# Kernel tuning notes

Measured on AMD Instinct MI355X. Metric: run time of the kernel, lower is better.

## Reference

```python
import jax, jax.numpy as jnp
import numpy as np

N_DIS = 5000
N_GEN = 20000
N = N_DIS + N_GEN
E = 400000
N_MIRNA = 2000
EMB = 128
HID = 64


def setup_inputs() -> dict:
    key = jax.random.key(0)
    ks = jax.random.split(key, 20)
    def g(k, shape, scale=0.05):
        return jax.random.normal(k, shape, dtype=jnp.float32) * scale
    return {
        'd_features': g(ks[0], (N_DIS, 383), 1.0),
        'g_features': g(ks[1], (N_GEN, 4395), 1.0),
        'miRNA_dis': jax.random.uniform(ks[2], (N_MIRNA, N_DIS), dtype=jnp.float32),
        'gene_dis': jax.random.uniform(ks[3], (N_GEN, N_DIS), dtype=jnp.float32),
        'Wd': g(ks[4], (383, EMB)),
        'bd': jnp.zeros((EMB,), jnp.float32),
        'Wg': g(ks[5], (4395, EMB)),
        'bg': jnp.zeros((EMB,), jnp.float32),
        'W1': g(ks[6], (N_MIRNA, EMB)),
        'W4': g(ks[7], (N_DIS, EMB)),
        'Ws1': g(ks[8], (EMB, HID)),
        'Wn1': g(ks[9], (EMB, HID)),
        'b1': jnp.zeros((HID,), jnp.float32),
        'Ws2': g(ks[10], (HID, HID)),
        'Wn2': g(ks[11], (HID, HID)),
        'b2': jnp.zeros((HID,), jnp.float32),
        'src': jax.random.randint(ks[12], (E,), 0, N, dtype=jnp.int32),
        'dst': jax.random.randint(ks[13], (E,), 0, N, dtype=jnp.int32),
    }


def _sage_mean(h, src, dst, Ws, Wn, b):
    # DGL SAGEConv 'mean': fc_self(h) + fc_neigh(mean over in-neighbors) + bias
    msg = h[src]                                            # [E, d] gather
    agg = jax.ops.segment_sum(msg, dst, num_segments=N)     # [N, d] scatter-add
    deg = jax.ops.segment_sum(jnp.ones((dst.shape[0],), h.dtype), dst, num_segments=N)
    neigh = agg / jnp.maximum(deg, 1.0)[:, None]            # mean (zero-deg -> 0)
    return h @ Ws + neigh @ Wn + b


def reference(d_features, g_features, miRNA_dis, gene_dis, Wd, bd, Wg, bg,
              W1, W4, Ws1, Wn1, b1, Ws2, Wn2, b2, src, dst):
    # CrossCompressUnit outputs used by forward: A2 = M1^T W1, B1 = M2 W4
    A2 = miRNA_dis.T @ W1          # [N_DIS, EMB]
    B1 = gene_dis @ W4             # [N_GEN, EMB]
    # Node embeddings (dropout is identity at inference; torch.no_grad block)
    h_dis = 0.9 * (d_features @ Wd + bd) + 0.1 * A2   # [N_DIS, EMB]
    h_gen = 0.9 * (g_features @ Wg + bg) + 0.1 * B1   # [N_GEN, EMB]
    h = jnp.concatenate([h_dis, h_gen], axis=0)        # [N, EMB]
    h = _sage_mean(h, src, dst, Ws1, Wn1, b1)          # [N, 64]
    h = jax.nn.relu(h)
    h = _sage_mean(h, src, dst, Ws2, Wn2, b2)          # [N, 64]
    return h
```

## Files before the change

kernel.cpp:

```cpp
#include <hip/hip_runtime.h>

#define NDIS 5000
#define NGEN 20000
#define NTOT 25000
#define EDG  400000

typedef __attribute__((ext_vector_type(8))) short short8;
typedef __attribute__((ext_vector_type(4))) float f32x4;
typedef __attribute__((ext_vector_type(4), aligned(4))) float f32x4u;
typedef __attribute__((ext_vector_type(4))) unsigned int uint4v;
typedef __attribute__((ext_vector_type(2))) unsigned int uint2v;
typedef __attribute__((ext_vector_type(2), aligned(4))) unsigned int uint2a;

constexpr size_t AL(size_t x) { return (x + 255) & ~(size_t)255; }
constexpr size_t OFF_H0   = 0;
constexpr size_t OFF_PQ   = AL(OFF_H0  + (size_t)NTOT * 128 * 4);
constexpr size_t OFF_H1   = AL(OFF_PQ  + (size_t)NTOT * 128 * 4);
constexpr size_t OFF_DEG  = AL(OFF_H1  + (size_t)NTOT * 128 * 4);
constexpr size_t OFF_RS   = AL(OFF_DEG + (size_t)NTOT * 4);
constexpr size_t OFF_CUR  = AL(OFF_RS  + (size_t)(NTOT + 1) * 4);
constexpr size_t OFF_TMP  = AL(OFF_CUR + (size_t)NTOT * 4);
constexpr size_t OFF_BSUM = AL(OFF_TMP + (size_t)NTOT * 4);
constexpr size_t OFF_BOFF = AL(OFF_BSUM + 64 * 4);
constexpr size_t OFF_ESRC = AL(OFF_BOFF + 64 * 4);
constexpr size_t OFF_MIT  = AL(OFF_ESRC + (size_t)EDG * 4);
constexpr size_t OFF_BDIS = AL(OFF_MIT + (size_t)5000 * 2048 * 2);
constexpr size_t OFF_BGEN = AL(OFF_BDIS + (size_t)8 * 76 * 512 * 2);
constexpr size_t OFF_BS1  = AL(OFF_BGEN + (size_t)8 * 300 * 512 * 2);
constexpr size_t OFF_BS2  = AL(OFF_BS1 + (size_t)8 * 4 * 512 * 2);

__device__ __forceinline__ ushort f2bf(float f) {
    unsigned u = __float_as_uint(f);
    u += 0x7fffu + ((u >> 16) & 1u);
    return (ushort)(u >> 16);
}

__device__ __forceinline__ unsigned cvtpk(float a, float b) {
    unsigned r;
    asm("v_cvt_pk_bf16_f32 %0, %1, %2" : "=v"(r) : "v"(a), "v"(b));
    return r;
}

__device__ __forceinline__ void MFMA(f32x4& d, short8 a, short8 b) {
    asm volatile("v_mfma_f32_16x16x32_bf16 %0, %1, %2, %0"
                 : "+v"(d) : "v"(a), "v"(b));
}

struct TcvtIns { const float* p[9]; };

__global__ __launch_bounds__(256) void k_tcvt_multi(TcvtIns ins, char* ws,
                                                    const int* __restrict__ dst,
                                                    int* __restrict__ deg)
{
    constexpr int   TR[9]   = {383, 2000, 4395, 5000, 2000, 128, 128, 64, 64};
    constexpr int   TC[9]   = {128, 128, 128, 128, 5000, 64, 64, 64, 64};
    constexpr int   TKT[9]  = {76, 76, 300, 300, 2048 , 4, 4, 4, 4};
    constexpr int   TKO[9]  = {0, 12, 0, 140, 0, 0, 0, 0, 0};
    constexpr int   TRP[9]  = {384, 2048, 4480, 5120, 2048, 128, 128, 128, 128};
    constexpr int   TNOFF[9]= {0, 0, 0, 0, 0, 0, 64, 0, 64};
    constexpr int   TMODE[9]= {1, 1, 1, 1, 0, 1, 1, 1, 1};
    constexpr float TSC[9]  = {0.9f, 0.1f, 0.9f, 0.1f, 1.f, 1.f, 1.f, 1.f, 1.f};
    constexpr size_t TOUT[9]= {OFF_BDIS, OFF_BDIS, OFF_BGEN, OFF_BGEN, OFF_MIT,
                               OFF_BS1, OFF_BS1, OFF_BS2, OFF_BS2};
    constexpr int TNBX[9]   = {4, 4, 4, 4, 157, 2, 2, 2, 2};
    constexpr int PRE[10]   = {0, 48, 304, 864, 1504, 11552, 11560, 11568, 11576, 11584};

    int bid = blockIdx.x;
    if (bid >= 11584) {
        int e = (bid - 11584) * 256 + threadIdx.x;
        if (e < EDG) atomicAdd(&deg[dst[e]], 1);
        return;
    }
    int d = 0;
#pragma unroll
    for (int q = 1; q < 9; ++q) if (bid >= PRE[q]) d = q;
    int local = bid - PRE[d];
    int bx = local % TNBX[d], by = local / TNBX[d];
    const int R = TR[d], C = TC[d], KT = TKT[d], KO = TKO[d];
    const int Rp = TRP[d], noff = TNOFF[d];
    const float scale = TSC[d];
    const float* in = ins.p[d];
    ushort* out = (ushort*)(ws + TOUT[d]);

    __shared__ float t[32][33];
    int tx = threadIdx.x & 31, ty = threadIdx.x >> 5;
    int c0 = bx * 32, r0 = by * 32;
#pragma unroll
    for (int j = 0; j < 4; ++j) {
        int r = r0 + ty + j * 8, c = c0 + tx;
        t[ty + j * 8][tx] = (r < R && c < C) ? in[(size_t)r * C + c] : 0.f;
    }
    __syncthreads();
#pragma unroll
    for (int j = 0; j < 4; ++j) {
        int c = c0 + ty + j * 8, r = r0 + tx;
        if (c >= C || r >= Rp) continue;
        ushort bv = f2bf(scale * t[tx][ty + j * 8]);
        if (TMODE[d] == 0) {
            out[(size_t)c * KT + r] = bv;
        } else {
            int n = noff + c, k = r;
            out[(size_t)((n >> 4) * KT + KO + (k >> 5)) * 512 +
                ((k >> 3) & 3) * 128 + (n & 15) * 8 + (k & 7)] = bv;
        }
    }
}

template<int A2MODE, bool ATOMIC>
__global__ __launch_bounds__(256, 2) void gemm_st(
    const float* __restrict__ A1, int lda1, int K1, int nst1,
    const void* __restrict__ A2v, int lda2, int K2, int nst2,
    const ushort* __restrict__ Bf, int KT,
    float* __restrict__ C, int M, const float* __restrict__ bias)
{
    __shared__ ushort lds0[64 * 128];
    __shared__ ushort lds1[64 * 128];
    const int tid  = threadIdx.x;
    const int lane = tid & 63;
    const int w    = tid >> 6;
    const int fr = lane & 15, kq = lane >> 4;
    const int bm0 = blockIdx.x * 64;

    const int NSTT = nst1 + nst2;
    const int per = (NSTT + gridDim.y - 1) / gridDim.y;
    const int s0 = blockIdx.y * per;
    const int s1 = min(NSTT, s0 + per);
    const int NT = s1 - s0;
    if (NT <= 0) return;

    f32x4 acc[4][2];
#pragma unroll
    for (int i = 0; i < 4; ++i) { acc[i][0] = {0.f,0.f,0.f,0.f}; acc[i][1] = {0.f,0.f,0.f,0.f}; }

    uint4v faA[8], faB[8];
    short8 Breg0[4][2], Breg1[4][2];

    const int srow = w * 16 + (lane >> 5);
    const int scol = lane & 31;

    auto issueA = [&](int stg, uint4v* fa) {
        const bool r1 = (A2MODE == 0) || (stg < nst1);
#pragma unroll
        for (int i = 0; i < 8; ++i) {
            int r = bm0 + srow + i * 2;
            if (r > M - 1) r = M - 1;
            if (r1) {
                const int kb = stg << 7;
                const int k = kb + scol * 4;
                const float* p = A1 + (size_t)r * lda1 + k;
                if (kb + 128 <= K1) {
                    fa[i] = __builtin_bit_cast(uint4v, *(const f32x4u*)p);
                } else {
                    f32x4 v;
#pragma unroll
                    for (int e = 0; e < 4; ++e) v[e] = (k + e < K1) ? p[e] : 0.f;
                    fa[i] = __builtin_bit_cast(uint4v, v);
                }
            } else if (A2MODE == 1) {
                const int kb = (stg - nst1) << 7;
                const int kc = kb + scol * 4;
                const float* p = (const float*)A2v + (size_t)r * lda2 + kc;
                if (kb + 128 <= K2) {
                    fa[i] = __builtin_bit_cast(uint4v, *(const f32x4u*)p);
                } else {
                    f32x4 v;
#pragma unroll
                    for (int e = 0; e < 4; ++e) v[e] = (kc + e < K2) ? p[e] : 0.f;
                    fa[i] = __builtin_bit_cast(uint4v, v);
                }
            } else {
                const int kc = ((stg - nst1) << 7) + scol * 4;
                uint2a v = *(const uint2a*)((const ushort*)A2v + (size_t)r * lda2 + kc);
                fa[i][0] = v[0]; fa[i][1] = v[1];
            }
        }
    };
    auto issueB = [&](int stg, short8 (*BR)[2]) {
#pragma unroll
        for (int ks = 0; ks < 4; ++ks)
#pragma unroll
            for (int nf = 0; nf < 2; ++nf)
                BR[ks][nf] = *(const short8*)(
                    Bf + (size_t)((w * 2 + nf) * KT + stg * 4 + ks) * 512 + lane * 8);
    };
    auto writeT = [&](int stg, const uint4v* fa, ushort* buf) {
        const bool cvt = (A2MODE != 2) || (stg < nst1);
        const int G = scol >> 1, h = lane & 1;
#pragma unroll
        for (int i = 0; i < 8; ++i) {
            int r = srow + i * 2;
            const size_t off = (size_t)r * 256 + ((G ^ (r & 7)) << 4) + h * 8;
            uint2v d;
            if (cvt) {
                f32x4 v = __builtin_bit_cast(f32x4, fa[i]);
                d[0] = cvtpk(v[0], v[1]);
                d[1] = cvtpk(v[2], v[3]);
            } else {
                d[0] = fa[i][0]; d[1] = fa[i][1];
            }
            *(uint2v*)((char*)buf + off) = d;
        }
    };

#define PHASE(T, BR, LDSC, FAW, LDSW)                                        \
    {                                                                        \
        const int x7 = fr & 7;                                               \
        _Pragma("unroll")                                                    \
        for (int ks = 0; ks < 4; ++ks) {                                     \
            short8 af[4];                                                    \
            _Pragma("unroll")                                                \
            for (int mf = 0; mf < 4; ++mf)                                   \
                af[mf] = *(const short8*)&LDSC[fr * 128 + mf * 2048 +        \
                                              (((ks * 4 + kq) ^ x7) << 3)];  \
            _Pragma("unroll")                                                \
            for (int mf = 0; mf < 4; ++mf) {                                 \
                MFMA(acc[mf][0], af[mf], BR[ks][0]);                         \
                MFMA(acc[mf][1], af[mf], BR[ks][1]);                         \
            }                                                                \
        }                                                                    \
        if ((T) + 2 < NT) issueB(s0 + (T) + 2, BR);                          \
        __builtin_amdgcn_s_barrier();                                        \
        if ((T) + 1 < NT) {                                                  \
            writeT(s0 + (T) + 1, FAW, LDSW);                                 \
            if ((T) + 3 < NT) issueA(s0 + (T) + 3, FAW);                     \
            asm volatile("s_waitcnt lgkmcnt(0)" ::: "memory");               \
            __builtin_amdgcn_s_barrier();                                    \
        }                                                                    \
    }

    issueA(s0, faA); issueB(s0, Breg0);
    if (NT > 1) { issueA(s0 + 1, faB); issueB(s0 + 1, Breg1); }
    writeT(s0, faA, lds0);
    if (NT > 2) issueA(s0 + 2, faA);
    asm volatile("s_waitcnt lgkmcnt(0)" ::: "memory");
    __builtin_amdgcn_s_barrier();

    for (int t = 0; t < NT; t += 2) {
        PHASE(t, Breg0, lds0, faB, lds1);
        if (t + 1 < NT) PHASE(t + 1, Breg1, lds1, faA, lds0);
    }
#undef PHASE

    asm volatile("s_nop 7\n\ts_nop 7\n\ts_nop 7" ::: "memory");
#pragma unroll
    for (int mf = 0; mf < 4; ++mf)
#pragma unroll
        for (int nf = 0; nf < 2; ++nf)
#pragma unroll
            for (int r = 0; r < 4; ++r) {
                int row = bm0 + mf * 16 + kq * 4 + r;
                if (row < M) {
                    int col = w * 32 + nf * 16 + fr;
                    if (ATOMIC) {
                        atomicAdd(&C[(size_t)row * 128 + col], acc[mf][nf][r]);
                    } else {
                        float v = acc[mf][nf][r];
                        if (col < 64) v += bias[col];
                        C[(size_t)row * 128 + col] = v;
                    }
                }
            }
}

__global__ void k_binit(float* __restrict__ h0, const float* __restrict__ bd,
                        const float* __restrict__ bg) {
    int i = blockIdx.x * 256 + threadIdx.x;
    if (i >= NTOT * 128) return;
    int col = i & 127;
    h0[i] = 0.9f * ((i >> 7) < NDIS ? bd[col] : bg[col]);
}

__global__ __launch_bounds__(1024) void k_scan1(const int* __restrict__ deg,
                                                int* __restrict__ tmp,
                                                int* __restrict__ bsum, int n) {
    __shared__ int wsum[16];
    int t = threadIdx.x, lane = t & 63, wid = t >> 6;
    int i = blockIdx.x * 1024 + t;
    int v = (i < n) ? deg[i] : 0;
    int x = v;
#pragma unroll
    for (int off = 1; off < 64; off <<= 1) {
        int y = __shfl_up(x, off, 64);
        if (lane >= off) x += y;
    }
    if (lane == 63) wsum[wid] = x;
    __syncthreads();
    if (wid == 0) {
        int s = (lane < 16) ? wsum[lane] : 0;
#pragma unroll
        for (int off = 1; off < 16; off <<= 1) {
            int y = __shfl_up(s, off, 64);
            if (lane >= off) s += y;
        }
        if (lane < 16) wsum[lane] = s;
    }
    __syncthreads();
    int incl = x + (wid > 0 ? wsum[wid - 1] : 0);
    if (i < n) tmp[i] = incl;
    if (t == 1023) bsum[blockIdx.x] = incl;
}

__global__ void k_scan2(const int* __restrict__ bsum, int* __restrict__ boff, int nb) {
    int t = threadIdx.x;
    int v = (t < nb) ? bsum[t] : 0;
    int x = v;
#pragma unroll
    for (int off = 1; off < 64; off <<= 1) {
        int y = __shfl_up(x, off, 64);
        if (t >= off) x += y;
    }
    if (t < nb) boff[t] = x - v;
}

__global__ __launch_bounds__(1024) void k_scan3(const int* __restrict__ deg,
                                                const int* __restrict__ tmp,
                                                const int* __restrict__ boff,
                                                int* __restrict__ rs,
                                                int* __restrict__ cursor, int n) {
    int i = blockIdx.x * 1024 + threadIdx.x;
    if (i == 0) rs[0] = 0;
    if (i < n) {
        int v = tmp[i] + boff[blockIdx.x];
        rs[i + 1] = v;
        cursor[i] = v - deg[i];
    }
}

__global__ void k_fill(const int* __restrict__ src, const int* __restrict__ dst,
                       int* __restrict__ cursor, int* __restrict__ esrc, int E) {
    int e = blockIdx.x * blockDim.x + threadIdx.x;
    if (e < E) {
        int pos = atomicAdd(&cursor[dst[e]], 1);
        esrc[pos] = src[e];
    }
}

__global__ __launch_bounds__(64) void k_agg(const float* __restrict__ PQ,
                                            const int* __restrict__ rs,
                                            const int* __restrict__ esrc,
                                            float* __restrict__ out, int ldout, int relu)
{
    int n = blockIdx.x, t = threadIdx.x;
    int s0 = rs[n], s1 = rs[n + 1];
    float a0 = 0.f, a1 = 0.f, a2 = 0.f, a3 = 0.f;
    int i = s0;
    for (; i + 4 <= s1; i += 4) {
        int e0 = esrc[i], e1 = esrc[i + 1], e2 = esrc[i + 2], e3 = esrc[i + 3];
        a0 += PQ[(size_t)e0 * 128 + 64 + t];
        a1 += PQ[(size_t)e1 * 128 + 64 + t];
        a2 += PQ[(size_t)e2 * 128 + 64 + t];
        a3 += PQ[(size_t)e3 * 128 + 64 + t];
    }
    for (; i < s1; ++i) a0 += PQ[(size_t)esrc[i] * 128 + 64 + t];
    float s = (a0 + a1) + (a2 + a3);
    float dg = (float)(s1 - s0);
    s /= fmaxf(dg, 1.f);
    float v = PQ[(size_t)n * 128 + t] + s;
    if (relu) v = fmaxf(v, 0.f);
    out[(size_t)n * ldout + t] = v;
}

extern "C" void kernel_launch(void* const* d_in, const int* in_sizes, int n_in,
                              void* d_out, int out_size, void* d_ws, size_t ws_size,
                              hipStream_t stream)
{
    const float* d_features = (const float*)d_in[0];
    const float* g_features = (const float*)d_in[1];
    const float* miRNA_dis  = (const float*)d_in[2];
    const float* gene_dis   = (const float*)d_in[3];
    const float* Wd  = (const float*)d_in[4];
    const float* bd  = (const float*)d_in[5];
    const float* Wg  = (const float*)d_in[6];
    const float* bg  = (const float*)d_in[7];
    const float* W1  = (const float*)d_in[8];
    const float* W4  = (const float*)d_in[9];
    const float* Ws1 = (const float*)d_in[10];
    const float* Wn1 = (const float*)d_in[11];
    const float* b1  = (const float*)d_in[12];
    const float* Ws2 = (const float*)d_in[13];
    const float* Wn2 = (const float*)d_in[14];
    const float* b2  = (const float*)d_in[15];
    const int* src = (const int*)d_in[16];
    const int* dst = (const int*)d_in[17];
    (void)in_sizes; (void)n_in; (void)out_size; (void)ws_size;

    char* ws = (char*)d_ws;
    float*  h0   = (float*)(ws + OFF_H0);
    float*  PQ   = (float*)(ws + OFF_PQ);
    float*  h1   = (float*)(ws + OFF_H1);
    int*    deg  = (int*)(ws + OFF_DEG);
    int*    rs   = (int*)(ws + OFF_RS);
    int*    cur  = (int*)(ws + OFF_CUR);
    int*    tmp  = (int*)(ws + OFF_TMP);
    int*    bsum = (int*)(ws + OFF_BSUM);
    int*    boff = (int*)(ws + OFF_BOFF);
    int*    esrc = (int*)(ws + OFF_ESRC);
    ushort* miT  = (ushort*)(ws + OFF_MIT);
    ushort* Bdis = (ushort*)(ws + OFF_BDIS);
    ushort* Bgen = (ushort*)(ws + OFF_BGEN);
    ushort* Bs1  = (ushort*)(ws + OFF_BS1);
    ushort* Bs2  = (ushort*)(ws + OFF_BS2);

    hipMemsetAsync(deg, 0, (size_t)NTOT * 4, stream);
    hipMemsetAsync(h1, 0, (size_t)NTOT * 128 * 4, stream);

    TcvtIns ins;
    ins.p[0] = Wd;  ins.p[1] = W1;  ins.p[2] = Wg;  ins.p[3] = W4;
    ins.p[4] = miRNA_dis; ins.p[5] = Ws1; ins.p[6] = Wn1; ins.p[7] = Ws2; ins.p[8] = Wn2;
    k_tcvt_multi<<<11584 + 1563, 256, 0, stream>>>(ins, ws, dst, deg);

    k_scan1<<<25, 1024, 0, stream>>>(deg, tmp, bsum, NTOT);
    k_scan2<<<1, 64, 0, stream>>>(bsum, boff, 25);
    k_scan3<<<25, 1024, 0, stream>>>(deg, tmp, boff, rs, cur, NTOT);
    k_fill<<<(EDG + 255) / 256, 256, 0, stream>>>(src, dst, cur, esrc, EDG);

    k_binit<<<(NTOT * 128 + 255) / 256, 256, 0, stream>>>(h0, bd, bg);
    gemm_st<2, true><<<dim3(79, 5), 256, 0, stream>>>(
        d_features, 383, 383, 3,
        miT, 2048, 2048, 16, Bdis, 76, h0, NDIS, nullptr);
    gemm_st<1, true><<<dim3(313, 4), 256, 0, stream>>>(
        g_features, 4395, 4395, 35,
        gene_dis, 5000, 5000, 40, Bgen, 300,
        h0 + (size_t)NDIS * 128, NGEN, nullptr);

    gemm_st<0, false><<<dim3(391, 1), 256, 0, stream>>>(
        h0, 128, 128, 1, nullptr, 0, 0, 0, Bs1, 4, PQ, NTOT, b1);
    k_agg<<<NTOT, 64, 0, stream>>>(PQ, rs, esrc, h1, 128, 1);

    gemm_st<0, false><<<dim3(391, 1), 256, 0, stream>>>(
        h1, 128, 128, 1, nullptr, 0, 0, 0, Bs2, 4, PQ, NTOT, b2);
    k_agg<<<NTOT, 64, 0, stream>>>(PQ, rs, esrc, (float*)d_out, 64, 0);
}
```

Measured before the change: 351.6 us.

## Double GEMM K-stage depth and replace double-buffered LDS pipeline with single buffer

The GEMM kernel now takes a templated K-step count, so the big feature GEMMs process 256-wide K stages (half as many barriers and stages), with the B-fragment packing and padding widened to match. The ping-pong LDS buffers and two-deep prefetch are replaced by a single LDS buffer with a simpler load–write–compute loop that prefetches only one stage ahead. This trims per-stage synchronisation overhead and LDS footprint, but it loses the explicit overlap of global loads with compute, needs more registers for the wider prefetch, and pads more zero K columns.

```diff
diff --git a/kernel.cpp b/kernel.cpp
--- a/kernel.cpp
+++ b/kernel.cpp
@@ -25,8 +25,8 @@
 constexpr size_t OFF_ESRC = AL(OFF_BOFF + 64 * 4);
 constexpr size_t OFF_MIT  = AL(OFF_ESRC + (size_t)EDG * 4);
 constexpr size_t OFF_BDIS = AL(OFF_MIT + (size_t)5000 * 2048 * 2);
-constexpr size_t OFF_BGEN = AL(OFF_BDIS + (size_t)8 * 76 * 512 * 2);
-constexpr size_t OFF_BS1  = AL(OFF_BGEN + (size_t)8 * 300 * 512 * 2);
+constexpr size_t OFF_BGEN = AL(OFF_BDIS + (size_t)8 * 80 * 512 * 2);
+constexpr size_t OFF_BS1  = AL(OFF_BGEN + (size_t)8 * 304 * 512 * 2);
 constexpr size_t OFF_BS2  = AL(OFF_BS1 + (size_t)8 * 4 * 512 * 2);
 
 __device__ __forceinline__ ushort f2bf(float f) {
@@ -54,20 +54,20 @@
 {
     constexpr int   TR[9]   = {383, 2000, 4395, 5000, 2000, 128, 128, 64, 64};
     constexpr int   TC[9]   = {128, 128, 128, 128, 5000, 64, 64, 64, 64};
-    constexpr int   TKT[9]  = {76, 76, 300, 300, 2048 , 4, 4, 4, 4};
-    constexpr int   TKO[9]  = {0, 12, 0, 140, 0, 0, 0, 0, 0};
-    constexpr int   TRP[9]  = {384, 2048, 4480, 5120, 2048, 128, 128, 128, 128};
+    constexpr int   TKT[9]  = {80, 80, 304, 304, 2048 , 4, 4, 4, 4};
+    constexpr int   TKO[9]  = {0, 16, 0, 144, 0, 0, 0, 0, 0};
+    constexpr int   TRP[9]  = {512, 2048, 4608, 5120, 2048, 128, 128, 128, 128};
     constexpr int   TNOFF[9]= {0, 0, 0, 0, 0, 0, 64, 0, 64};
     constexpr int   TMODE[9]= {1, 1, 1, 1, 0, 1, 1, 1, 1};
     constexpr float TSC[9]  = {0.9f, 0.1f, 0.9f, 0.1f, 1.f, 1.f, 1.f, 1.f, 1.f};
     constexpr size_t TOUT[9]= {OFF_BDIS, OFF_BDIS, OFF_BGEN, OFF_BGEN, OFF_MIT,
                                OFF_BS1, OFF_BS1, OFF_BS2, OFF_BS2};
     constexpr int TNBX[9]   = {4, 4, 4, 4, 157, 2, 2, 2, 2};
-    constexpr int PRE[10]   = {0, 48, 304, 864, 1504, 11552, 11560, 11568, 11576, 11584};
+    constexpr int PRE[10]   = {0, 64, 320, 896, 1536, 11584, 11592, 11600, 11608, 11616};
 
     int bid = blockIdx.x;
-    if (bid >= 11584) {
-        int e = (bid - 11584) * 256 + threadIdx.x;
+    if (bid >= 11616) {
+        int e = (bid - 11616) * 256 + threadIdx.x;
         if (e < EDG) atomicAdd(&deg[dst[e]], 1);
         return;
     }
@@ -106,140 +106,144 @@
     }
 }
 
-template<int A2MODE, bool ATOMIC>
+template<int A2MODE, bool ATOMIC, int NKS>
 __global__ __launch_bounds__(256, 2) void gemm_st(
     const float* __restrict__ A1, int lda1, int K1, int nst1,
     const void* __restrict__ A2v, int lda2, int K2, int nst2,
     const ushort* __restrict__ Bf, int KT,
     float* __restrict__ C, int M, const float* __restrict__ bias)
 {
-    __shared__ ushort lds0[64 * 128];
-    __shared__ ushort lds1[64 * 128];
+    constexpr int SUP = NKS * 32;
+    constexpr int JPR = NKS / 4;
+    __shared__ ushort lds[64 * SUP];
     const int tid  = threadIdx.x;
     const int lane = tid & 63;
     const int w    = tid >> 6;
     const int fr = lane & 15, kq = lane >> 4;
     const int bm0 = blockIdx.x * 64;
+    const int grp  = tid >> 5;
+    const int scol = lane & 31;
 
     const int NSTT = nst1 + nst2;
     const int per = (NSTT + gridDim.y - 1) / gridDim.y;
     const int s0 = blockIdx.y * per;
     const int s1 = min(NSTT, s0 + per);
-    const int NT = s1 - s0;
-    if (NT <= 0) return;
+    if (s0 >= s1) return;
 
     f32x4 acc[4][2];
 #pragma unroll
     for (int i = 0; i < 4; ++i) { acc[i][0] = {0.f,0.f,0.f,0.f}; acc[i][1] = {0.f,0.f,0.f,0.f}; }
 
-    uint4v faA[8], faB[8];
-    short8 Breg0[4][2], Breg1[4][2];
-
-    const int srow = w * 16 + (lane >> 5);
-    const int scol = lane & 31;
-
-    auto issueA = [&](int stg, uint4v* fa) {
+    uint4v fa[8 * JPR];
+    short8 Br[NKS][2];
+
+    auto issueA = [&](int stg) {
         const bool r1 = (A2MODE == 0) || (stg < nst1);
 #pragma unroll
         for (int i = 0; i < 8; ++i) {
-            int r = bm0 + srow + i * 2;
+            int r = bm0 + grp + i * 8;
             if (r > M - 1) r = M - 1;
             if (r1) {
-                const int kb = stg << 7;
-                const int k = kb + scol * 4;
-                const float* p = A1 + (size_t)r * lda1 + k;
-                if (kb + 128 <= K1) {
-                    fa[i] = __builtin_bit_cast(uint4v, *(const f32x4u*)p);
-                } else {
-                    f32x4 v;
-#pragma unroll
-                    for (int e = 0; e < 4; ++e) v[e] = (k + e < K1) ? p[e] : 0.f;
-                    fa[i] = __builtin_bit_cast(uint4v, v);
+                const int kb = stg * SUP;
+#pragma unroll
+                for (int j = 0; j < JPR; ++j) {
+                    const int k = kb + j * 128 + scol * 4;
+                    const float* p = A1 + (size_t)r * lda1 + k;
+                    if (kb + SUP <= K1) {
+                        fa[i * JPR + j] = __builtin_bit_cast(uint4v, *(const f32x4u*)p);
+                    } else {
+                        f32x4 v;
+#pragma unroll
+                        for (int e = 0; e < 4; ++e) v[e] = (k + e < K1) ? p[e] : 0.f;
+                        fa[i * JPR + j] = __builtin_bit_cast(uint4v, v);
+                    }
                 }
             } else if (A2MODE == 1) {
-                const int kb = (stg - nst1) << 7;
-                const int kc = kb + scol * 4;
-                const float* p = (const float*)A2v + (size_t)r * lda2 + kc;
-                if (kb + 128 <= K2) {
-                    fa[i] = __builtin_bit_cast(uint4v, *(const f32x4u*)p);
-                } else {
-                    f32x4 v;
-#pragma unroll
-                    for (int e = 0; e < 4; ++e) v[e] = (kc + e < K2) ? p[e] : 0.f;
-                    fa[i] = __builtin_bit_cast(uint4v, v);
+                const int kb = (stg - nst1) * SUP;
+#pragma unroll
+                for (int j = 0; j < JPR; ++j) {
+                    const int kc = kb + j * 128 + scol * 4;
+                    const float* p = (const float*)A2v + (size_t)r * lda2 + kc;
+                    if (kb + SUP <= K2) {
+                        fa[i * JPR + j] = __builtin_bit_cast(uint4v, *(const f32x4u*)p);
+                    } else {
+                        f32x4 v;
+#pragma unroll
+                        for (int e = 0; e < 4; ++e) v[e] = (kc + e < K2) ? p[e] : 0.f;
+                        fa[i * JPR + j] = __builtin_bit_cast(uint4v, v);
+                    }
                 }
             } else {
-                const int kc = ((stg - nst1) << 7) + scol * 4;
-                uint2a v = *(const uint2a*)((const ushort*)A2v + (size_t)r * lda2 + kc);
-                fa[i][0] = v[0]; fa[i][1] = v[1];
+                const int kb = (stg - nst1) * SUP;
+#pragma unroll
+                for (int j = 0; j < JPR; ++j) {
+                    const int kc = kb + j * 128 + scol * 4;
+                    uint2a v = *(const uint2a*)((const ushort*)A2v + (size_t)r * lda2 + kc);
+                    fa[i * JPR + j][0] = v[0];
+                    fa[i * JPR + j][1] = v[1];
+                }
             }
         }
     };
-    auto issueB = [&](int stg, short8 (*BR)[2]) {
-#pragma unroll
-        for (int ks = 0; ks < 4; ++ks)
+    auto issueB = [&](int stg) {
+#pragma unroll
+        for (int ks = 0; ks < NKS; ++ks)
 #pragma unroll
             for (int nf = 0; nf < 2; ++nf)
-                BR[ks][nf] = *(const short8*)(
-                    Bf + (size_t)((w * 2 + nf) * KT + stg * 4 + ks) * 512 + lane * 8);
+                Br[ks][nf] = *(const short8*)(
+                    Bf + (size_t)((w * 2 + nf) * KT + stg * NKS + ks) * 512 + lane * 8);
     };
-    auto writeT = [&](int stg, const uint4v* fa, ushort* buf) {
+    auto writeT = [&](int stg) {
         const bool cvt = (A2MODE != 2) || (stg < nst1);
-        const int G = scol >> 1, h = lane & 1;
 #pragma unroll
         for (int i = 0; i < 8; ++i) {
-            int r = srow + i * 2;
-            const size_t off = (size_t)r * 256 + ((G ^ (r & 7)) << 4) + h * 8;
-            uint2v d;
-            if (cvt) {
-                f32x4 v = __builtin_bit_cast(f32x4, fa[i]);
-                d[0] = cvtpk(v[0], v[1]);
-                d[1] = cvtpk(v[2], v[3]);
-            } else {
-                d[0] = fa[i][0]; d[1] = fa[i][1];
+            const int rL = grp + i * 8;
+#pragma unroll
+            for (int j = 0; j < JPR; ++j) {
+                const int slot16 = (scol >> 1) + j * 16;
+                const size_t off = (size_t)rL * (SUP * 2) +
+                                   ((slot16 ^ (rL & 7)) << 4) + (scol & 1) * 8;
+                uint2v d;
+                if (cvt) {
+                    f32x4 v = __builtin_bit_cast(f32x4, fa[i * JPR + j]);
+                    d[0] = cvtpk(v[0], v[1]);
+                    d[1] = cvtpk(v[2], v[3]);
+                } else {
+                    d[0] = fa[i * JPR + j][0];
+                    d[1] = fa[i * JPR + j][1];
+                }
+                *(uint2v*)((char*)lds + off) = d;
             }
-            *(uint2v*)((char*)buf + off) = d;
         }
     };
-
-#define PHASE(T, BR, LDSC, FAW, LDSW)                                        \
-    {                                                                        \
-        const int x7 = fr & 7;                                               \
-        _Pragma("unroll")                                                    \
-        for (int ks = 0; ks < 4; ++ks) {                                     \
-            short8 af[4];                                                    \
-            _Pragma("unroll")                                                \
-            for (int mf = 0; mf < 4; ++mf)                                   \
-                af[mf] = *(const short8*)&LDSC[fr * 128 + mf * 2048 +        \
-                                              (((ks * 4 + kq) ^ x7) << 3)];  \
-            _Pragma("unroll")                                                \
-            for (int mf = 0; mf < 4; ++mf) {                                 \
-                MFMA(acc[mf][0], af[mf], BR[ks][0]);                         \
-                MFMA(acc[mf][1], af[mf], BR[ks][1]);                         \
-            }                                                                \
-        }                                                                    \
-        if ((T) + 2 < NT) issueB(s0 + (T) + 2, BR);                          \
-        __builtin_amdgcn_s_barrier();                                        \
-        if ((T) + 1 < NT) {                                                  \
-            writeT(s0 + (T) + 1, FAW, LDSW);                                 \
-            if ((T) + 3 < NT) issueA(s0 + (T) + 3, FAW);                     \
-            asm volatile("s_waitcnt lgkmcnt(0)" ::: "memory");               \
-            __builtin_amdgcn_s_barrier();                                    \
-        }                                                                    \
-    }
-
-    issueA(s0, faA); issueB(s0, Breg0);
-    if (NT > 1) { issueA(s0 + 1, faB); issueB(s0 + 1, Breg1); }
-    writeT(s0, faA, lds0);
-    if (NT > 2) issueA(s0 + 2, faA);
-    asm volatile("s_waitcnt lgkmcnt(0)" ::: "memory");
-    __builtin_amdgcn_s_barrier();
-
-    for (int t = 0; t < NT; t += 2) {
-        PHASE(t, Breg0, lds0, faB, lds1);
-        if (t + 1 < NT) PHASE(t + 1, Breg1, lds1, faA, lds0);
-    }
-#undef PHASE
+    auto compute = [&]() {
+        const int x7 = fr & 7;
+#pragma unroll
+        for (int ks = 0; ks < NKS; ++ks) {
+            short8 af[4];
+#pragma unroll
+            for (int mf = 0; mf < 4; ++mf)
+                af[mf] = *(const short8*)((char*)lds +
+                    (size_t)(mf * 16 + fr) * (SUP * 2) +
+                    (((ks * 4 + kq) ^ x7) << 4));
+#pragma unroll
+            for (int mf = 0; mf < 4; ++mf) {
+                MFMA(acc[mf][0], af[mf], Br[ks][0]);
+                MFMA(acc[mf][1], af[mf], Br[ks][1]);
+            }
+        }
+    };
+
+    issueA(s0); issueB(s0);
+    for (int t = s0; t < s1; ++t) {
+        writeT(t);
+        if (t + 1 < s1) issueA(t + 1);
+        asm volatile("s_waitcnt lgkmcnt(0)" ::: "memory");
+        __builtin_amdgcn_s_barrier();
+        compute();
+        if (t + 1 < s1) issueB(t + 1);
+        __builtin_amdgcn_s_barrier();
+    }
 
     asm volatile("s_nop 7\n\ts_nop 7\n\ts_nop 7" ::: "memory");
 #pragma unroll
@@ -407,7 +411,7 @@
     TcvtIns ins;
     ins.p[0] = Wd;  ins.p[1] = W1;  ins.p[2] = Wg;  ins.p[3] = W4;
     ins.p[4] = miRNA_dis; ins.p[5] = Ws1; ins.p[6] = Wn1; ins.p[7] = Ws2; ins.p[8] = Wn2;
-    k_tcvt_multi<<<11584 + 1563, 256, 0, stream>>>(ins, ws, dst, deg);
+    k_tcvt_multi<<<11616 + 1563, 256, 0, stream>>>(ins, ws, dst, deg);
 
     k_scan1<<<25, 1024, 0, stream>>>(deg, tmp, bsum, NTOT);
     k_scan2<<<1, 64, 0, stream>>>(bsum, boff, 25);
@@ -415,19 +419,19 @@
     k_fill<<<(EDG + 255) / 256, 256, 0, stream>>>(src, dst, cur, esrc, EDG);
 
     k_binit<<<(NTOT * 128 + 255) / 256, 256, 0, stream>>>(h0, bd, bg);
-    gemm_st<2, true><<<dim3(79, 5), 256, 0, stream>>>(
-        d_features, 383, 383, 3,
-        miT, 2048, 2048, 16, Bdis, 76, h0, NDIS, nullptr);
-    gemm_st<1, true><<<dim3(313, 4), 256, 0, stream>>>(
-        g_features, 4395, 4395, 35,
-        gene_dis, 5000, 5000, 40, Bgen, 300,
+    gemm_st<2, true, 8><<<dim3(79, 5), 256, 0, stream>>>(
+        d_features, 383, 383, 2,
+        miT, 2048, 2048, 8, Bdis, 80, h0, NDIS, nullptr);
+    gemm_st<1, true, 8><<<dim3(313, 4), 256, 0, stream>>>(
+        g_features, 4395, 4395, 18,
+        gene_dis, 5000, 5000, 20, Bgen, 304,
         h0 + (size_t)NDIS * 128, NGEN, nullptr);
 
-    gemm_st<0, false><<<dim3(391, 1), 256, 0, stream>>>(
+    gemm_st<0, false, 4><<<dim3(391, 1), 256, 0, stream>>>(
         h0, 128, 128, 1, nullptr, 0, 0, 0, Bs1, 4, PQ, NTOT, b1);
     k_agg<<<NTOT, 64, 0, stream>>>(PQ, rs, esrc, h1, 128, 1);
 
-    gemm_st<0, false><<<dim3(391, 1), 256, 0, stream>>>(
+    gemm_st<0, false, 4><<<dim3(391, 1), 256, 0, stream>>>(
         h1, 128, 128, 1, nullptr, 0, 0, 0, Bs2, 4, PQ, NTOT, b2);
     k_agg<<<NTOT, 64, 0, stream>>>(PQ, rs, esrc, (float*)d_out, 64, 0);
 }
```

Result: no change. 351.7 us (median of 2 runs) (+0.0%).
